# Kernel optimization log

Measured on AMD Instinct MI355X. Metric: run time of the kernel, lower is better.

## Reference

```python
import jax, jax.numpy as jnp
import numpy as np

NU, NI, D, LAYERS, NNZ = 50000, 50000, 256, 2, 400000
N = NU + NI
LEAKY_ALPHA = 0.2  # tf.nn.leaky_relu default


def setup_inputs() -> dict:
    key = jax.random.key(0)
    ks = jax.random.split(key, 32)
    inp = {}
    inp["initial_ebs"] = jax.random.normal(ks[0], (N, D), jnp.float32) * 0.1
    for i, nm in enumerate(["W_side_u", "W_dot_u", "W_side_i", "W_dot_i"]):
        inp[nm] = jax.random.normal(ks[1 + i], (LAYERS, D, D), jnp.float32) / np.float32(np.sqrt(D))
    vi = 5
    for ent, ne in (("u", NU), ("i", NI)):
        for mat in ("LI", "L"):
            inp[f"{mat}_vals_{ent}"] = jax.random.uniform(ks[vi], (NNZ,), jnp.float32); vi += 1
            inp[f"{mat}_rows_{ent}"] = jnp.sort(jax.random.randint(ks[vi], (NNZ,), 0, ne, jnp.int32)); vi += 1
            inp[f"{mat}_cols_{ent}"] = jax.random.randint(ks[vi], (NNZ,), 0, N, jnp.int32); vi += 1
    return inp


def _spmm(rows, cols, vals, ebs, n_rows):
    # sparse [n_rows, N] @ dense [N, D] via gather + segment-sum
    return jax.ops.segment_sum(vals[:, None] * ebs[cols], rows, num_segments=n_rows)


def reference(initial_ebs, W_side_u, W_dot_u, W_side_i, W_dot_i,
              LI_vals_u, L_vals_u, LI_vals_i, L_vals_i,
              LI_rows_u, LI_cols_u, L_rows_u, L_cols_u,
              LI_rows_i, LI_cols_i, L_rows_i, L_cols_i):
    ebs = initial_ebs
    layers_ebs = []
    for l in range(LAYERS):
        # entity 'u': rows [0, NU)
        li_u = _spmm(LI_rows_u, LI_cols_u, LI_vals_u, ebs, NU)
        l_u = _spmm(L_rows_u, L_cols_u, L_vals_u, ebs, NU)
        fold_u = jax.nn.leaky_relu(li_u @ W_side_u[l] + (l_u * ebs[:NU]) @ W_dot_u[l], LEAKY_ALPHA)
        # entity 'i': rows [NU, N)
        li_i = _spmm(LI_rows_i, LI_cols_i, LI_vals_i, ebs, NI)
        l_i = _spmm(L_rows_i, L_cols_i, L_vals_i, ebs, NI)
        fold_i = jax.nn.leaky_relu(li_i @ W_side_i[l] + (l_i * ebs[NU:]) @ W_dot_i[l], LEAKY_ALPHA)
        ebs = jnp.concatenate([fold_u, fold_i], axis=0)  # [N, D]
        layers_ebs.append(ebs)
    return jnp.concatenate(layers_ebs, axis=0)  # [LAYERS*N, D]
```

## Files before the change

kernel.cpp:

```cpp
#include <hip/hip_runtime.h>

#define NUQ 50000
#define NIQ 50000
#define DQ 256
#define NTOT 100000
#define LALPHA 0.2f
#define GPE 782

typedef __attribute__((ext_vector_type(8))) __bf16 bf16x8;
typedef __attribute__((ext_vector_type(4))) float floatx4;
typedef __attribute__((ext_vector_type(8))) unsigned short ushort8;

__device__ __forceinline__ float b2f(unsigned short u) {
    unsigned int x = ((unsigned int)u) << 16;
    return __builtin_bit_cast(float, x);
}
__device__ __forceinline__ unsigned short f2b(float f) {
    unsigned int u = __builtin_bit_cast(unsigned int, f);
    u = u + 0x7FFFu + ((u >> 16) & 1u);
    return (unsigned short)(u >> 16);
}

#define GLD_LDS16(g, l)                                                        \
    __builtin_amdgcn_global_load_lds(                                          \
        (const __attribute__((address_space(1))) void*)(g),                    \
        (__attribute__((address_space(3))) void*)(l), 16, 0, 0)

__global__ __launch_bounds__(256) void build_rowptr(
    const int* __restrict__ rows, int nnz, int* __restrict__ rptr, int n_rows)
{
    int e = blockIdx.x * 256 + threadIdx.x;
    if (e > nnz) return;
    int prev = (e == 0)   ? -1     : rows[e - 1];
    int cur  = (e == nnz) ? n_rows : rows[e];
    for (int r = prev + 1; r <= cur; ++r) rptr[r] = e;
}

__global__ __launch_bounds__(256) void cvt_f32_bf16(
    const float* __restrict__ in, unsigned short* __restrict__ out, int n4)
{
    int i = blockIdx.x * 256 + threadIdx.x;
    if (i >= n4) return;
    float4 v = ((const float4*)in)[i];
    ushort4 o;
    o.x = f2b(v.x); o.y = f2b(v.y); o.z = f2b(v.z); o.w = f2b(v.w);
    ((ushort4*)out)[i] = o;
}

__global__ __launch_bounds__(256) void build_bt(
    const float* __restrict__ Ws_u, const float* __restrict__ Wd_u,
    const float* __restrict__ Ws_i, const float* __restrict__ Wd_i,
    unsigned short* __restrict__ Bt)
{
    int idx = blockIdx.x * 256 + threadIdx.x;
    int k   = idx & 511;
    int n   = (idx >> 9) & 255;
    int buf = idx >> 17;
    int l = buf >> 1, e = buf & 1;
    const float* Wside = e ? Ws_i : Ws_u;
    const float* Wdot  = e ? Wd_i : Wd_u;
    float v = (k < 256) ? Wside[((size_t)l * 256 + k)       * 256 + n]
                        : Wdot [((size_t)l * 256 + (k-256)) * 256 + n];
    Bt[idx] = f2b(v);
}

__global__ __launch_bounds__(256) void spmm_merged_v3(
    const int* __restrict__ rpA_u, const int* __restrict__ cA_u, const float* __restrict__ vA_u,
    const int* __restrict__ rpB_u, const int* __restrict__ cB_u, const float* __restrict__ vB_u,
    const int* __restrict__ rpA_i, const int* __restrict__ cA_i, const float* __restrict__ vA_i,
    const int* __restrict__ rpB_i, const int* __restrict__ cB_i, const float* __restrict__ vB_i,
    const unsigned short* __restrict__ src,
    unsigned short* __restrict__ out)
{
    const int wave = threadIdx.x >> 6;
    const int lane = threadIdx.x & 63;
    const int r    = __builtin_amdgcn_readfirstlane(blockIdx.x * 4 + wave);
    const bool isI = (r >= NUQ);
    const int  row = isI ? (r - NUQ) : r;

    const int*   rpA = isI ? rpA_i : rpA_u;
    const int*   cAp = isI ? cA_i  : cA_u;
    const float* vAp = isI ? vA_i  : vA_u;
    const int*   rpB = isI ? rpB_i : rpB_u;
    const int*   cBp = isI ? cB_i  : cB_u;
    const float* vBp = isI ? vB_i  : vB_u;

    const int sA = rpA[row], eA = rpA[row + 1];
    const int sB = rpB[row], eB = rpB[row + 1];

    const int half = lane >> 5;
    const int li   = lane & 31;

    float accA[8] = {0.f, 0.f, 0.f, 0.f, 0.f, 0.f, 0.f, 0.f};
    float accB[8] = {0.f, 0.f, 0.f, 0.f, 0.f, 0.f, 0.f, 0.f};

    int baseA = sA, baseB = sB;
    while (baseA < eA || baseB < eB) {
        int cntA = eA - baseA; cntA = cntA < 0 ? 0 : (cntA > 64 ? 64 : cntA);
        int cntB = eB - baseB; cntB = cntB < 0 ? 0 : (cntB > 64 ? 64 : cntB);
        int mycA = 0; float myvA = 0.f;
        if (lane < cntA) { mycA = cAp[baseA + lane]; myvA = vAp[baseA + lane]; }
        int mycB = 0; float myvB = 0.f;
        if (lane < cntB) { mycB = cBp[baseB + lane]; myvB = vBp[baseB + lane]; }
        const int mx = cntA > cntB ? cntA : cntB;
        #pragma unroll 2
        for (int e = 0; e < mx; e += 2) {
            if (e < cntA) {
                const int   c = __shfl(mycA, e + half, 64);
                const float v = __shfl(myvA, e + half, 64);
                const ushort8 s = *(const ushort8*)(src + (size_t)c * DQ + li * 8);
                #pragma unroll
                for (int j = 0; j < 8; ++j) accA[j] = fmaf(v, b2f(s[j]), accA[j]);
            }
            if (e < cntB) {
                const int   c = __shfl(mycB, e + half, 64);
                const float v = __shfl(myvB, e + half, 64);
                const ushort8 s = *(const ushort8*)(src + (size_t)c * DQ + li * 8);
                #pragma unroll
                for (int j = 0; j < 8; ++j) accB[j] = fmaf(v, b2f(s[j]), accB[j]);
            }
        }
        baseA += 64; baseB += 64;
    }

    #pragma unroll
    for (int j = 0; j < 8; ++j) accA[j] += __shfl_xor(accA[j], 32, 64);
    #pragma unroll
    for (int j = 0; j < 8; ++j) accB[j] += __shfl_xor(accB[j], 32, 64);

    float vo[8];
    if (half == 0) {
        #pragma unroll
        for (int j = 0; j < 8; ++j) vo[j] = accA[j];
    } else {
        const ushort8 m = *(const ushort8*)(src + (size_t)r * DQ + li * 8);
        #pragma unroll
        for (int j = 0; j < 8; ++j) vo[j] = accB[j] * b2f(m[j]);
    }
    ushort8 o;
    #pragma unroll
    for (int j = 0; j < 8; ++j) o[j] = f2b(vo[j]);
    *(ushort8*)(out + (size_t)r * 512 + half * 256 + li * 8) = o;
}

__global__ __launch_bounds__(256) void gemm_mfma_leaky_v3(
    const unsigned short* __restrict__ A,
    const unsigned short* __restrict__ Btl,
    float* __restrict__ out,
    unsigned short* __restrict__ ebs,
    const int wb)
{
    __shared__ unsigned short As[2][2048];
    __shared__ unsigned short Bs[2][8192];

    const int tid  = threadIdx.x;
    const int lane = tid & 63;
    const int w    = tid >> 6;
    const int ent  = (blockIdx.x >= GPE) ? 1 : 0;
    const int bx   = blockIdx.x - ent * GPE;
    const int row0 = ent * NUQ + bx * 64;
    const int Mend = ent * NUQ + NUQ;
    const unsigned short* Bt = Btl + (size_t)ent * 131072;

    const int mA  = ((tid >> 6) << 4) | (tid & 15);
    const int kbA = (tid >> 4) & 3;
    int grs = row0 + mA; if (grs >= Mend) grs = Mend - 1;
    const unsigned short* gA = A + (size_t)grs * 512 + kbA * 8;
    const int ldsA = w * 512;

    const unsigned short* gB[4];
    #pragma unroll
    for (int j = 0; j < 4; ++j) {
        int t = j * 256 + tid;
        int n = ((t >> 6) << 4) | (t & 15);
        gB[j] = Bt + (size_t)n * 512 + ((t >> 4) & 3) * 8;
    }
    const int ldsB = w * 512;

    const int lr  = lane >> 4;
    const int lc  = lane & 15;
    const int gmb = (w & 1) * 2;
    const int gnb = (w >> 1) * 8;

    floatx4 acc[2][8] = {};

    GLD_LDS16(gA, &As[0][ldsA]);
    #pragma unroll
    for (int j = 0; j < 4; ++j) GLD_LDS16(gB[j], &Bs[0][j * 2048 + ldsB]);
    GLD_LDS16(gA + 32, &As[1][ldsA]);
    #pragma unroll
    for (int j = 0; j < 4; ++j) GLD_LDS16(gB[j] + 32, &Bs[1][j * 2048 + ldsB]);

    for (int kt = 0; kt < 16; ++kt) {
        const int cur = kt & 1;
        if (kt < 15) asm volatile("s_waitcnt vmcnt(5)" ::: "memory");
        else         asm volatile("s_waitcnt vmcnt(0)" ::: "memory");
        __builtin_amdgcn_s_barrier();

        bf16x8 af[2], bfr[8];
        #pragma unroll
        for (int tm = 0; tm < 2; ++tm)
            af[tm] = *(const bf16x8*)&As[cur][(gmb + tm) * 512 + lr * 128 + lc * 8];
        #pragma unroll
        for (int tn = 0; tn < 8; ++tn)
            bfr[tn] = *(const bf16x8*)&Bs[cur][(gnb + tn) * 512 + lr * 128 + lc * 8];

        asm volatile("s_waitcnt lgkmcnt(0)" ::: "memory");
        __builtin_amdgcn_s_barrier();

        if (kt < 14) {
            const int ko = (kt + 2) * 32;
            GLD_LDS16(gA + ko, &As[cur][ldsA]);
            #pragma unroll
            for (int j = 0; j < 4; ++j)
                GLD_LDS16(gB[j] + ko, &Bs[cur][j * 2048 + ldsB]);
        }

        __builtin_amdgcn_s_setprio(1);
        #pragma unroll
        for (int tm = 0; tm < 2; ++tm)
            #pragma unroll
            for (int tn = 0; tn < 8; ++tn)
                acc[tm][tn] = __builtin_amdgcn_mfma_f32_16x16x32_bf16(
                    af[tm], bfr[tn], acc[tm][tn], 0, 0, 0);
        __builtin_amdgcn_s_setprio(0);
    }

    const int m_off = (w & 1) * 32;
    const int n_off = (w >> 1) * 128;
    #pragma unroll
    for (int tm = 0; tm < 2; ++tm) {
        #pragma unroll
        for (int rr = 0; rr < 4; ++rr) {
            const int gr = row0 + m_off + tm * 16 + lr * 4 + rr;
            if (gr >= Mend) continue;
            float*          orow = out + (size_t)gr * 256;
            unsigned short* brow = ebs + (size_t)gr * 256;
            #pragma unroll
            for (int tn = 0; tn < 8; ++tn) {
                const int gc = n_off + tn * 16 + lc;
                float v = acc[tm][tn][rr];
                v = v > 0.f ? v : LALPHA * v;
                orow[gc] = v;
                if (wb) brow[gc] = f2b(v);
            }
        }
    }
}

extern "C" void kernel_launch(void* const* d_in, const int* in_sizes, int n_in,
                              void* d_out, int out_size, void* d_ws, size_t ws_size,
                              hipStream_t stream) {
    const float* ebs0      = (const float*)d_in[0];
    const float* W_side_u  = (const float*)d_in[1];
    const float* W_dot_u   = (const float*)d_in[2];
    const float* W_side_i  = (const float*)d_in[3];
    const float* W_dot_i   = (const float*)d_in[4];
    const float* LI_vals_u = (const float*)d_in[5];
    const int*   LI_rows_u = (const int*)  d_in[6];
    const int*   LI_cols_u = (const int*)  d_in[7];
    const float* L_vals_u  = (const float*)d_in[8];
    const int*   L_rows_u  = (const int*)  d_in[9];
    const int*   L_cols_u  = (const int*)  d_in[10];
    const float* LI_vals_i = (const float*)d_in[11];
    const int*   LI_rows_i = (const int*)  d_in[12];
    const int*   LI_cols_i = (const int*)  d_in[13];
    const float* L_vals_i  = (const float*)d_in[14];
    const int*   L_rows_i  = (const int*)  d_in[15];
    const int*   L_cols_i  = (const int*)  d_in[16];

    float* out = (float*)d_out;

    unsigned short* Abuf   = (unsigned short*)d_ws;
    unsigned short* ebs_bf = (unsigned short*)((char*)d_ws + 102400000);
    unsigned short* Bt     = (unsigned short*)((char*)d_ws + 153600000);
    int* rp_LI_u = (int*)((char*)d_ws + 154648576);
    int* rp_L_u  = rp_LI_u + 50001;
    int* rp_LI_i = rp_L_u  + 50001;
    int* rp_L_i  = rp_LI_i + 50001;

    const int nnz_LI_u = in_sizes[5];
    const int nnz_L_u  = in_sizes[8];
    const int nnz_LI_i = in_sizes[11];
    const int nnz_L_i  = in_sizes[14];

    dim3 b256(256);
    build_rowptr<<<dim3((nnz_LI_u + 256) / 256), b256, 0, stream>>>(LI_rows_u, nnz_LI_u, rp_LI_u, NUQ);
    build_rowptr<<<dim3((nnz_L_u  + 256) / 256), b256, 0, stream>>>(L_rows_u,  nnz_L_u,  rp_L_u,  NUQ);
    build_rowptr<<<dim3((nnz_LI_i + 256) / 256), b256, 0, stream>>>(LI_rows_i, nnz_LI_i, rp_LI_i, NIQ);
    build_rowptr<<<dim3((nnz_L_i  + 256) / 256), b256, 0, stream>>>(L_rows_i,  nnz_L_i,  rp_L_i,  NIQ);
    build_bt<<<dim3(2048), b256, 0, stream>>>(W_side_u, W_dot_u, W_side_i, W_dot_i, Bt);
    cvt_f32_bf16<<<dim3(25000), b256, 0, stream>>>(ebs0, ebs_bf, NTOT * DQ / 4);

    dim3 sgrid(NTOT / 4);
    dim3 ggrid(2 * GPE);

    for (int l = 0; l < 2; ++l) {
        float* outl = out + (size_t)l * NTOT * DQ;
        spmm_merged_v3<<<sgrid, b256, 0, stream>>>(
            rp_LI_u, LI_cols_u, LI_vals_u, rp_L_u, L_cols_u, L_vals_u,
            rp_LI_i, LI_cols_i, LI_vals_i, rp_L_i, L_cols_i, L_vals_i,
            ebs_bf, Abuf);
        gemm_mfma_leaky_v3<<<ggrid, b256, 0, stream>>>(
            Abuf, Bt + (size_t)l * 2 * 131072, outl, ebs_bf, (l == 0) ? 1 : 0);
    }
}
```

Before: 706.5 us.

## Fuse SpMM gather into MFMA GEMM kernel via LDS-resident A tile

Merges the SpMM and GEMM kernels into one. Each block gathers its 64 rows of the concatenated [LI, L*ebs] operand straight into a swizzled 64x512 bf16 LDS tile, then runs the MFMA GEMM with leaky ReLU on it. This drops the global write and re-read of the intermediate A buffer and one launch per layer. Embeddings are now double-buffered (ebs0/ebs1) so one layer's gather never reads rows another block is overwriting. In exchange the B pipeline loses double buffering and waits on synchronous barriers. The 64 KB A tile plus the B tile also limit occupancy, and each wave gathers 16 rows one after another, so latency hiding during the gather may drop.

Measured after the change: 994.6 us. +40.8%, slower.

```diff
diff --git a/kernel.cpp b/kernel.cpp
--- a/kernel.cpp
+++ b/kernel.cpp
@@ -64,109 +64,105 @@
     Bt[idx] = f2b(v);
 }
 
-__global__ __launch_bounds__(256) void spmm_merged_v3(
+__global__ __launch_bounds__(256, 2) void fused_spmm_gemm(
     const int* __restrict__ rpA_u, const int* __restrict__ cA_u, const float* __restrict__ vA_u,
     const int* __restrict__ rpB_u, const int* __restrict__ cB_u, const float* __restrict__ vB_u,
     const int* __restrict__ rpA_i, const int* __restrict__ cA_i, const float* __restrict__ vA_i,
     const int* __restrict__ rpB_i, const int* __restrict__ cB_i, const float* __restrict__ vB_i,
     const unsigned short* __restrict__ src,
-    unsigned short* __restrict__ out)
-{
-    const int wave = threadIdx.x >> 6;
-    const int lane = threadIdx.x & 63;
-    const int r    = __builtin_amdgcn_readfirstlane(blockIdx.x * 4 + wave);
-    const bool isI = (r >= NUQ);
-    const int  row = isI ? (r - NUQ) : r;
-
-    const int*   rpA = isI ? rpA_i : rpA_u;
-    const int*   cAp = isI ? cA_i  : cA_u;
-    const float* vAp = isI ? vA_i  : vA_u;
-    const int*   rpB = isI ? rpB_i : rpB_u;
-    const int*   cBp = isI ? cB_i  : cB_u;
-    const float* vBp = isI ? vB_i  : vB_u;
-
-    const int sA = rpA[row], eA = rpA[row + 1];
-    const int sB = rpB[row], eB = rpB[row + 1];
-
-    const int half = lane >> 5;
-    const int li   = lane & 31;
-
-    float accA[8] = {0.f, 0.f, 0.f, 0.f, 0.f, 0.f, 0.f, 0.f};
-    float accB[8] = {0.f, 0.f, 0.f, 0.f, 0.f, 0.f, 0.f, 0.f};
-
-    int baseA = sA, baseB = sB;
-    while (baseA < eA || baseB < eB) {
-        int cntA = eA - baseA; cntA = cntA < 0 ? 0 : (cntA > 64 ? 64 : cntA);
-        int cntB = eB - baseB; cntB = cntB < 0 ? 0 : (cntB > 64 ? 64 : cntB);
-        int mycA = 0; float myvA = 0.f;
-        if (lane < cntA) { mycA = cAp[baseA + lane]; myvA = vAp[baseA + lane]; }
-        int mycB = 0; float myvB = 0.f;
-        if (lane < cntB) { mycB = cBp[baseB + lane]; myvB = vBp[baseB + lane]; }
-        const int mx = cntA > cntB ? cntA : cntB;
-        #pragma unroll 2
-        for (int e = 0; e < mx; e += 2) {
-            if (e < cntA) {
-                const int   c = __shfl(mycA, e + half, 64);
-                const float v = __shfl(myvA, e + half, 64);
-                const ushort8 s = *(const ushort8*)(src + (size_t)c * DQ + li * 8);
-                #pragma unroll
-                for (int j = 0; j < 8; ++j) accA[j] = fmaf(v, b2f(s[j]), accA[j]);
-            }
-            if (e < cntB) {
-                const int   c = __shfl(mycB, e + half, 64);
-                const float v = __shfl(myvB, e + half, 64);
-                const ushort8 s = *(const ushort8*)(src + (size_t)c * DQ + li * 8);
-                #pragma unroll
-                for (int j = 0; j < 8; ++j) accB[j] = fmaf(v, b2f(s[j]), accB[j]);
-            }
-        }
-        baseA += 64; baseB += 64;
-    }
-
-    #pragma unroll
-    for (int j = 0; j < 8; ++j) accA[j] += __shfl_xor(accA[j], 32, 64);
-    #pragma unroll
-    for (int j = 0; j < 8; ++j) accB[j] += __shfl_xor(accB[j], 32, 64);
-
-    float vo[8];
-    if (half == 0) {
-        #pragma unroll
-        for (int j = 0; j < 8; ++j) vo[j] = accA[j];
-    } else {
-        const ushort8 m = *(const ushort8*)(src + (size_t)r * DQ + li * 8);
-        #pragma unroll
-        for (int j = 0; j < 8; ++j) vo[j] = accB[j] * b2f(m[j]);
-    }
-    ushort8 o;
-    #pragma unroll
-    for (int j = 0; j < 8; ++j) o[j] = f2b(vo[j]);
-    *(ushort8*)(out + (size_t)r * 512 + half * 256 + li * 8) = o;
-}
-
-__global__ __launch_bounds__(256) void gemm_mfma_leaky_v3(
-    const unsigned short* __restrict__ A,
     const unsigned short* __restrict__ Btl,
     float* __restrict__ out,
-    unsigned short* __restrict__ ebs,
+    unsigned short* __restrict__ ebs_next,
     const int wb)
 {
-    __shared__ unsigned short As[2][2048];
-    __shared__ unsigned short Bs[2][8192];
+    __shared__ unsigned short A_lds[32768];
+    __shared__ unsigned short Bs[8192];
 
     const int tid  = threadIdx.x;
     const int lane = tid & 63;
     const int w    = tid >> 6;
+    const int wu   = __builtin_amdgcn_readfirstlane(w);
     const int ent  = (blockIdx.x >= GPE) ? 1 : 0;
     const int bx   = blockIdx.x - ent * GPE;
     const int row0 = ent * NUQ + bx * 64;
     const int Mend = ent * NUQ + NUQ;
     const unsigned short* Bt = Btl + (size_t)ent * 131072;
 
-    const int mA  = ((tid >> 6) << 4) | (tid & 15);
-    const int kbA = (tid >> 4) & 3;
-    int grs = row0 + mA; if (grs >= Mend) grs = Mend - 1;
-    const unsigned short* gA = A + (size_t)grs * 512 + kbA * 8;
-    const int ldsA = w * 512;
+    const int*   rpA = ent ? rpA_i : rpA_u;
+    const int*   cAp = ent ? cA_i  : cA_u;
+    const float* vAp = ent ? vA_i  : vA_u;
+    const int*   rpB = ent ? rpB_i : rpB_u;
+    const int*   cBp = ent ? cB_i  : cB_u;
+    const float* vBp = ent ? vB_i  : vB_u;
+
+    const int half = lane >> 5;
+    const int li   = lane & 31;
+
+    for (int rr = 0; rr < 16; ++rr) {
+        const int rl = wu * 16 + rr;
+        const int r  = row0 + rl;
+        const int widx = (rl * 512 + lane * 8) ^ ((rl & 7) << 3);
+
+        if (r >= Mend) {
+            ushort8 z = {0,0,0,0,0,0,0,0};
+            *(ushort8*)&A_lds[widx] = z;
+            continue;
+        }
+        const int row = r - ent * NUQ;
+        const int sA = rpA[row], eA = rpA[row + 1];
+        const int sB = rpB[row], eB = rpB[row + 1];
+
+        float accA[8] = {0.f,0.f,0.f,0.f,0.f,0.f,0.f,0.f};
+        float accB[8] = {0.f,0.f,0.f,0.f,0.f,0.f,0.f,0.f};
+
+        int baseA = sA, baseB = sB;
+        while (baseA < eA || baseB < eB) {
+            int cntA = eA - baseA; cntA = cntA < 0 ? 0 : (cntA > 64 ? 64 : cntA);
+            int cntB = eB - baseB; cntB = cntB < 0 ? 0 : (cntB > 64 ? 64 : cntB);
+            int mycA = 0; float myvA = 0.f;
+            if (lane < cntA) { mycA = cAp[baseA + lane]; myvA = vAp[baseA + lane]; }
+            int mycB = 0; float myvB = 0.f;
+            if (lane < cntB) { mycB = cBp[baseB + lane]; myvB = vBp[baseB + lane]; }
+            const int mx = cntA > cntB ? cntA : cntB;
+            #pragma unroll 4
+            for (int e = 0; e < mx; e += 2) {
+                if (e < cntA) {
+                    const int   c = __shfl(mycA, e + half, 64);
+                    const float v = __shfl(myvA, e + half, 64);
+                    const ushort8 s = *(const ushort8*)(src + (size_t)c * DQ + li * 8);
+                    #pragma unroll
+                    for (int j = 0; j < 8; ++j) accA[j] = fmaf(v, b2f(s[j]), accA[j]);
+                }
+                if (e < cntB) {
+                    const int   c = __shfl(mycB, e + half, 64);
+                    const float v = __shfl(myvB, e + half, 64);
+                    const ushort8 s = *(const ushort8*)(src + (size_t)c * DQ + li * 8);
+                    #pragma unroll
+                    for (int j = 0; j < 8; ++j) accB[j] = fmaf(v, b2f(s[j]), accB[j]);
+                }
+            }
+            baseA += 64; baseB += 64;
+        }
+
+        #pragma unroll
+        for (int j = 0; j < 8; ++j) accA[j] += __shfl_xor(accA[j], 32, 64);
+        #pragma unroll
+        for (int j = 0; j < 8; ++j) accB[j] += __shfl_xor(accB[j], 32, 64);
+
+        float vo[8];
+        if (half == 0) {
+            #pragma unroll
+            for (int j = 0; j < 8; ++j) vo[j] = accA[j];
+        } else {
+            const ushort8 m = *(const ushort8*)(src + (size_t)r * DQ + li * 8);
+            #pragma unroll
+            for (int j = 0; j < 8; ++j) vo[j] = accB[j] * b2f(m[j]);
+        }
+        ushort8 o;
+        #pragma unroll
+        for (int j = 0; j < 8; ++j) o[j] = f2b(vo[j]);
+        *(ushort8*)&A_lds[widx] = o;
+    }
 
     const unsigned short* gB[4];
     #pragma unroll
@@ -179,42 +175,30 @@
 
     const int lr  = lane >> 4;
     const int lc  = lane & 15;
-    const int gmb = (w & 1) * 2;
-    const int gnb = (w >> 1) * 8;
+    const int m_off = (w & 1) * 32;
+    const int n_off = (w >> 1) * 128;
+    const int gnb   = (w >> 1) * 8;
 
     floatx4 acc[2][8] = {};
 
-    GLD_LDS16(gA, &As[0][ldsA]);
-    #pragma unroll
-    for (int j = 0; j < 4; ++j) GLD_LDS16(gB[j], &Bs[0][j * 2048 + ldsB]);
-    GLD_LDS16(gA + 32, &As[1][ldsA]);
-    #pragma unroll
-    for (int j = 0; j < 4; ++j) GLD_LDS16(gB[j] + 32, &Bs[1][j * 2048 + ldsB]);
-
     for (int kt = 0; kt < 16; ++kt) {
-        const int cur = kt & 1;
-        if (kt < 15) asm volatile("s_waitcnt vmcnt(5)" ::: "memory");
-        else         asm volatile("s_waitcnt vmcnt(0)" ::: "memory");
-        __builtin_amdgcn_s_barrier();
+        const int ko = kt * 32;
+        #pragma unroll
+        for (int j = 0; j < 4; ++j)
+            GLD_LDS16(gB[j] + ko, &Bs[j * 2048 + ldsB]);
+        __syncthreads();
 
         bf16x8 af[2], bfr[8];
         #pragma unroll
-        for (int tm = 0; tm < 2; ++tm)
-            af[tm] = *(const bf16x8*)&As[cur][(gmb + tm) * 512 + lr * 128 + lc * 8];
+        for (int tm = 0; tm < 2; ++tm) {
+            const int m = m_off + tm * 16 + lc;
+            af[tm] = *(const bf16x8*)&A_lds[(m * 512 + ko + lr * 8) ^ ((m & 7) << 3)];
+        }
         #pragma unroll
         for (int tn = 0; tn < 8; ++tn)
-            bfr[tn] = *(const bf16x8*)&Bs[cur][(gnb + tn) * 512 + lr * 128 + lc * 8];
-
-        asm volatile("s_waitcnt lgkmcnt(0)" ::: "memory");
-        __builtin_amdgcn_s_barrier();
-
-        if (kt < 14) {
-            const int ko = (kt + 2) * 32;
-            GLD_LDS16(gA + ko, &As[cur][ldsA]);
-            #pragma unroll
-            for (int j = 0; j < 4; ++j)
-                GLD_LDS16(gB[j] + ko, &Bs[cur][j * 2048 + ldsB]);
-        }
+            bfr[tn] = *(const bf16x8*)&Bs[(gnb + tn) * 512 + lr * 128 + lc * 8];
+
+        __syncthreads();
 
         __builtin_amdgcn_s_setprio(1);
         #pragma unroll
@@ -226,16 +210,14 @@
         __builtin_amdgcn_s_setprio(0);
     }
 
-    const int m_off = (w & 1) * 32;
-    const int n_off = (w >> 1) * 128;
     #pragma unroll
     for (int tm = 0; tm < 2; ++tm) {
         #pragma unroll
         for (int rr = 0; rr < 4; ++rr) {
             const int gr = row0 + m_off + tm * 16 + lr * 4 + rr;
             if (gr >= Mend) continue;
-            float*          orow = out + (size_t)gr * 256;
-            unsigned short* brow = ebs + (size_t)gr * 256;
+            float*          orow = out      + (size_t)gr * 256;
+            unsigned short* brow = ebs_next + (size_t)gr * 256;
             #pragma unroll
             for (int tn = 0; tn < 8; ++tn) {
                 const int gc = n_off + tn * 16 + lc;
@@ -271,10 +253,10 @@
 
     float* out = (float*)d_out;
 
-    unsigned short* Abuf   = (unsigned short*)d_ws;
-    unsigned short* ebs_bf = (unsigned short*)((char*)d_ws + 102400000);
-    unsigned short* Bt     = (unsigned short*)((char*)d_ws + 153600000);
-    int* rp_LI_u = (int*)((char*)d_ws + 154648576);
+    unsigned short* ebs0_bf = (unsigned short*)d_ws;
+    unsigned short* ebs1_bf = (unsigned short*)((char*)d_ws + 51200000);
+    unsigned short* Bt      = (unsigned short*)((char*)d_ws + 102400000);
+    int* rp_LI_u = (int*)((char*)d_ws + 103448576);
     int* rp_L_u  = rp_LI_u + 50001;
     int* rp_LI_i = rp_L_u  + 50001;
     int* rp_L_i  = rp_LI_i + 50001;
@@ -290,18 +272,16 @@
     build_rowptr<<<dim3((nnz_LI_i + 256) / 256), b256, 0, stream>>>(LI_rows_i, nnz_LI_i, rp_LI_i, NIQ);
     build_rowptr<<<dim3((nnz_L_i  + 256) / 256), b256, 0, stream>>>(L_rows_i,  nnz_L_i,  rp_L_i,  NIQ);
     build_bt<<<dim3(2048), b256, 0, stream>>>(W_side_u, W_dot_u, W_side_i, W_dot_i, Bt);
-    cvt_f32_bf16<<<dim3(25000), b256, 0, stream>>>(ebs0, ebs_bf, NTOT * DQ / 4);
-
-    dim3 sgrid(NTOT / 4);
-    dim3 ggrid(2 * GPE);
+    cvt_f32_bf16<<<dim3(25000), b256, 0, stream>>>(ebs0, ebs0_bf, NTOT * DQ / 4);
+
+    dim3 fgrid(2 * GPE);
 
     for (int l = 0; l < 2; ++l) {
         float* outl = out + (size_t)l * NTOT * DQ;
-        spmm_merged_v3<<<sgrid, b256, 0, stream>>>(
+        const unsigned short* srcl = (l == 0) ? ebs0_bf : ebs1_bf;
+        fused_spmm_gemm<<<fgrid, b256, 0, stream>>>(
             rp_LI_u, LI_cols_u, LI_vals_u, rp_L_u, L_cols_u, L_vals_u,
             rp_LI_i, LI_cols_i, LI_vals_i, rp_L_i, L_cols_i, L_vals_i,
-            ebs_bf, Abuf);
-        gemm_mfma_leaky_v3<<<ggrid, b256, 0, stream>>>(
-            Abuf, Bt + (size_t)l * 2 * 131072, outl, ebs_bf, (l == 0) ? 1 : 0);
-    }
-}
+            srcl, Bt + (size_t)l * 2 * 131072, outl, ebs1_bf, (l == 0) ? 1 : 0);
+    }
+}
```
